# Performance work log

Measured on AMD Instinct MI355X. Metric: run time of the kernel, lower is better.

Reference implementation:

```python
import jax, jax.numpy as jnp
import numpy as np

N_NODES = 100000
M_HYPER = 50000
N_TOTAL = N_NODES + M_HYPER  # 150000
D_IN = 512
H_LAT = 256
N_CLASS = 40
NNZ = 4800000
NUM_LAYERS = 3


def setup_inputs() -> dict:
    key = jax.random.key(0)
    ks = jax.random.split(key, 8)
    X = jax.random.normal(ks[0], (N_TOTAL, D_IN), dtype=jnp.float32)
    W_red = jax.random.normal(ks[1], (D_IN, H_LAT), dtype=jnp.float32) / np.sqrt(D_IN)
    b_red = jax.random.normal(ks[2], (H_LAT,), dtype=jnp.float32) * 0.01
    W_cls = jax.random.normal(ks[3], (H_LAT, N_CLASS), dtype=jnp.float32) / np.sqrt(H_LAT)
    b_cls = jax.random.normal(ks[4], (N_CLASS,), dtype=jnp.float32) * 0.01
    # COO sparse normalized graph: value ~ 1/degree scale (avg_degree=32)
    edge_rows = jax.random.randint(ks[5], (NNZ,), 0, N_TOTAL, dtype=jnp.int32)
    edge_cols = jax.random.randint(ks[6], (NNZ,), 0, N_TOTAL, dtype=jnp.int32)
    edge_vals = jax.random.uniform(ks[7], (NNZ,), dtype=jnp.float32) * (1.0 / 32.0)
    return {
        "X": X, "W_red": W_red, "b_red": b_red,
        "W_cls": W_cls, "b_cls": b_cls,
        "edge_vals": edge_vals, "edge_rows": edge_rows, "edge_cols": edge_cols,
    }


def _spmm(edge_vals, edge_rows, edge_cols, emb):
    # out[r] = sum_{e: rows[e]==r} vals[e] * emb[cols[e]]
    msgs = edge_vals[:, None] * emb[edge_cols]  # [NNZ, H]
    return jax.ops.segment_sum(msgs, edge_rows, num_segments=N_TOTAL)


def reference(X, W_red, b_red, W_cls, b_cls, edge_vals, edge_rows, edge_cols):
    # reduction layer (dropout is identity in eval mode)
    emb = X @ W_red + b_red  # [N_TOTAL, H]
    # LightGCN-style propagation with running mean over layer outputs
    acc = emb
    cur = emb
    for _ in range(NUM_LAYERS):
        cur = _spmm(edge_vals, edge_rows, edge_cols, cur)
        acc = acc + cur
    out = acc / (NUM_LAYERS + 1)
    nodes = out[:N_NODES]  # split: nodes vs hyperedges
    Z = nodes @ W_cls + b_cls  # [N_NODES, C]
    return jax.nn.log_softmax(Z, axis=1)
```

## Files before the change

### kernel.cpp

```cpp
#include <hip/hip_runtime.h>

#define N_NODES 100000
#define M_HYPER 50000
#define N_TOTAL 150000
#define D_IN    512
#define H_LAT   256
#define N_CLASS 40
#define NNZ_E   4800000
#define CNT_PAD 151552
#define BK      128
#define BROWS   256
#define NB      ((N_TOTAL + BROWS - 1) / BROWS)
#define CH      4096
#define CLS_FB  16

#define S_EMB   16.0f
#define SP_OUT  8.0f
#define INV1    (1.0f / 128.0f)
#define INV2    (1.0f / 1024.0f)
#define INV3    (1.0f / 8192.0f)

typedef float  floatx4 __attribute__((ext_vector_type(4)));
typedef float  floatx2 __attribute__((ext_vector_type(2)));
typedef __bf16 bf16x8  __attribute__((ext_vector_type(8)));

__device__ __forceinline__ unsigned short bf16_rne(float f) {
    unsigned u = __float_as_uint(f);
    return (unsigned short)((u + 0x7FFFu + ((u >> 16) & 1u)) >> 16);
}
__device__ __forceinline__ float blo(unsigned w) { return __uint_as_float(w << 16); }
__device__ __forceinline__ float bhi(unsigned w) { return __uint_as_float(w & 0xFFFF0000u); }

__device__ __forceinline__ unsigned pack4fp8(float f0, float f1, float f2, float f3) {
    int d = __builtin_amdgcn_cvt_pk_fp8_f32(f0, f1, 0, false);
    d = __builtin_amdgcn_cvt_pk_fp8_f32(f2, f3, d, true);
    return (unsigned)d;
}

__global__ void __launch_bounds__(256) prep_wt_kernel(const float* __restrict__ W,
                                                      unsigned short* __restrict__ WT) {
    int t = blockIdx.x * 256 + threadIdx.x;
    if (t < D_IN * H_LAT) {
        int k = t >> 8;
        int n = t & 255;
        WT[n * D_IN + k] = bf16_rne(W[t]);
    }
}

__global__ void __launch_bounds__(256, 2) gemm1_kernel(const float* __restrict__ X,
                                                       const unsigned short* __restrict__ WT,
                                                       const float* __restrict__ brd,
                                                       unsigned short* __restrict__ emb,
                                                       unsigned char* __restrict__ emb8) {
    __shared__ __align__(16) unsigned short smem[64 * (H_LAT + 8)];
    unsigned short (*As)[BK + 8]    = (unsigned short (*)[BK + 8])smem;
    unsigned short (*Cs)[H_LAT + 8] = (unsigned short (*)[H_LAT + 8])smem;

    int tid  = threadIdx.x;
    int wv   = tid >> 6;
    int lane = tid & 63;
    int l16  = lane & 15;
    int quad = lane >> 4;
    int row0 = blockIdx.x * 64;

    int cst = (tid & 31) << 2;
    int rst = tid >> 5;
    const float* xbase = X + cst;

    float4 pf[8];
#pragma unroll
    for (int j = 0; j < 8; ++j) {
        int gr = min(row0 + rst + 8 * j, N_TOTAL - 1);
        pf[j] = *(const float4*)(xbase + (size_t)gr * D_IN);
    }

    floatx4 acc[4][4];
#pragma unroll
    for (int a = 0; a < 4; ++a)
#pragma unroll
        for (int b = 0; b < 4; ++b) acc[a][b] = (floatx4)0.f;

#pragma unroll 1
    for (int k0 = 0; k0 < D_IN; k0 += BK) {
#pragma unroll
        for (int j = 0; j < 8; ++j) {
            ushort4 u;
            u.x = bf16_rne(pf[j].x); u.y = bf16_rne(pf[j].y);
            u.z = bf16_rne(pf[j].z); u.w = bf16_rne(pf[j].w);
            *(ushort4*)(&As[rst + 8 * j][cst]) = u;
        }
        __syncthreads();

        bf16x8 bw[4][4];
#pragma unroll
        for (int s = 0; s < 4; ++s)
#pragma unroll
            for (int ct = 0; ct < 4; ++ct) {
                int col = wv * 64 + ct * 16 + l16;
                bw[s][ct] = *(const bf16x8*)(WT + (size_t)col * D_IN + k0 + s * 32 + quad * 8);
            }
        asm volatile("" ::: "memory");

        if (k0 + BK < D_IN) {
#pragma unroll
            for (int j = 0; j < 8; ++j) {
                int gr = min(row0 + rst + 8 * j, N_TOTAL - 1);
                pf[j] = *(const float4*)(xbase + (size_t)gr * D_IN + k0 + BK);
            }
        }
        asm volatile("" ::: "memory");

#pragma unroll
        for (int s = 0; s < 4; ++s) {
            int ks = s * 32;
            bf16x8 af[4];
#pragma unroll
            for (int rt = 0; rt < 4; ++rt)
                af[rt] = *(const bf16x8*)(&As[rt * 16 + l16][ks + quad * 8]);
#pragma unroll
            for (int ct = 0; ct < 4; ++ct) {
#pragma unroll
                for (int rt = 0; rt < 4; ++rt)
                    acc[rt][ct] = __builtin_amdgcn_mfma_f32_16x16x32_bf16(af[rt], bw[s][ct], acc[rt][ct], 0, 0, 0);
            }
        }
        __syncthreads();
    }

#pragma unroll
    for (int ct = 0; ct < 4; ++ct) {
        int col = wv * 64 + ct * 16 + l16;
        float bias = brd[col];
#pragma unroll
        for (int rt = 0; rt < 4; ++rt)
#pragma unroll
            for (int r = 0; r < 4; ++r)
                Cs[rt * 16 + quad * 4 + r][col] = bf16_rne(acc[rt][ct][r] + bias);
    }
    __syncthreads();

    int nbf = N_NODES - row0;
#pragma unroll
    for (int j = 0; j < 8; ++j) {
        int idx = tid + 256 * j;
        int r = idx >> 5;
        int cq = (idx & 31) * 8;
        if (r < nbf)
            *(uint4*)(emb + (size_t)(row0 + r) * H_LAT + cq) = *(const uint4*)(&Cs[r][cq]);
    }
#pragma unroll
    for (int j = 0; j < 4; ++j) {
        int idx = tid + 256 * j;
        int r = idx >> 4;
        int cq = (idx & 15) * 16;
        if (row0 + r < N_TOTAL) {
            const unsigned short* s = &Cs[r][cq];
            uint4 w0 = *(const uint4*)s;
            uint4 w1 = *(const uint4*)(s + 8);
            uint4 o;
            o.x = pack4fp8(S_EMB * blo(w0.x), S_EMB * bhi(w0.x), S_EMB * blo(w0.y), S_EMB * bhi(w0.y));
            o.y = pack4fp8(S_EMB * blo(w0.z), S_EMB * bhi(w0.z), S_EMB * blo(w0.w), S_EMB * bhi(w0.w));
            o.z = pack4fp8(S_EMB * blo(w1.x), S_EMB * bhi(w1.x), S_EMB * blo(w1.y), S_EMB * bhi(w1.y));
            o.w = pack4fp8(S_EMB * blo(w1.z), S_EMB * bhi(w1.z), S_EMB * blo(w1.w), S_EMB * bhi(w1.w));
            *(uint4*)(emb8 + (size_t)(row0 + r) * H_LAT + cq) = o;
        }
    }
}

__global__ void __launch_bounds__(256) bcnt_kernel(const int* __restrict__ rows,
                                                   int* __restrict__ bcnt) {
    __shared__ int h[NB];
    int tid = threadIdx.x;
    for (int i = tid; i < NB; i += 256) h[i] = 0;
    __syncthreads();
    long base = (long)blockIdx.x * (CH / 4);
    const int4* r4 = (const int4*)rows;
#pragma unroll
    for (int j = 0; j < 4; ++j) {
        long e = base + j * 256 + tid;
        if (e < NNZ_E / 4) {
            int4 r = r4[e];
            atomicAdd(&h[r.x >> 8], 1);
            atomicAdd(&h[r.y >> 8], 1);
            atomicAdd(&h[r.z >> 8], 1);
            atomicAdd(&h[r.w >> 8], 1);
        }
    }
    __syncthreads();
    for (int i = tid; i < NB; i += 256) {
        int c = h[i];
        if (c) atomicAdd(&bcnt[i], c);
    }
}

__global__ void __launch_bounds__(1024) bscan_kernel(const int* __restrict__ bcnt,
                                                     int* __restrict__ bptr,
                                                     int* __restrict__ bucket_fill) {
    __shared__ int ws[16];
    int tid = threadIdx.x;
    int lane = tid & 63, wid = tid >> 6;
    int v = (tid < NB) ? bcnt[tid] : 0;
    int s = v;
#pragma unroll
    for (int d = 1; d < 64; d <<= 1) {
        int o = __shfl_up(s, d);
        if (lane >= d) s += o;
    }
    if (lane == 63) ws[wid] = s;
    __syncthreads();
    if (wid == 0) {
        int w = (lane < 16) ? ws[lane] : 0;
#pragma unroll
        for (int d = 1; d < 16; d <<= 1) {
            int o = __shfl_up(w, d);
            if (lane >= d) w += o;
        }
        if (lane < 16) ws[lane] = w;
    }
    __syncthreads();
    int excl = s - v + ((wid > 0) ? ws[wid - 1] : 0);
    if (tid < NB) {
        bptr[tid] = excl;
        bucket_fill[tid] = excl;
    }
    if (tid == 0) bptr[NB] = NNZ_E;
}

__global__ void __launch_bounds__(256) binA_kernel(const int* __restrict__ rows,
                                                   const int* __restrict__ cols,
                                                   const float* __restrict__ vals,
                                                   int* __restrict__ bucket_fill,
                                                   int2* __restrict__ binned) {
    __shared__ int hist[NB];
    int tid = threadIdx.x;
    long base = (long)blockIdx.x * CH;
    for (int i = tid; i < NB; i += 256) hist[i] = 0;
    __syncthreads();

    int mybkt[16];
    int myrl[16];
#pragma unroll
    for (int j = 0; j < 16; ++j) {
        long e = base + j * 256 + tid;
        int b = -1, rl = 0;
        if (e < NNZ_E) {
            int r = rows[e];
            b = r >> 8;
            rl = r & 255;
            atomicAdd(&hist[b], 1);
        }
        mybkt[j] = b; myrl[j] = rl;
    }
    __syncthreads();
    for (int b = tid; b < NB; b += 256) {
        int c = hist[b];
        int g = 0;
        if (c > 0) g = atomicAdd(&bucket_fill[b], c);
        hist[b] = g;
    }
    __syncthreads();
#pragma unroll
    for (int j = 0; j < 16; ++j) {
        long e = base + j * 256 + tid;
        if (e < NNZ_E) {
            int b = mybkt[j];
            int pos = atomicAdd(&hist[b], 1);
            int c = cols[e];
            float v = vals[e];
            binned[pos] = make_int2(c | (myrl[j] << 18), __float_as_int(v));
        }
    }
}

__global__ void __launch_bounds__(256) binB_kernel(const int* __restrict__ bptr,
                                                   const int2* __restrict__ binned,
                                                   int* __restrict__ row_ptr,
                                                   int2* __restrict__ csr_ev) {
    __shared__ int lh[256];
    __shared__ int lofs[256];
    __shared__ int wsum[4];
    int b = blockIdx.x;
    int tid = threadIdx.x;
    int s = bptr[b], e = bptr[b + 1];

    lh[tid] = 0;
    __syncthreads();
    for (int t = s + tid; t < e; t += 256)
        atomicAdd(&lh[((unsigned)binned[t].x) >> 18], 1);
    __syncthreads();

    int v = lh[tid];
    int lane = tid & 63, wid = tid >> 6;
    int sc = v;
#pragma unroll
    for (int d = 1; d < 64; d <<= 1) {
        int o = __shfl_up(sc, d);
        if (lane >= d) sc += o;
    }
    if (lane == 63) wsum[wid] = sc;
    __syncthreads();
    int woff = 0;
    if (wid > 0) woff = wsum[0];
    if (wid > 1) woff += wsum[1];
    if (wid > 2) woff += wsum[2];
    int excl = sc - v + woff;
    lofs[tid] = s + excl;
    row_ptr[b * BROWS + tid] = s + excl;
    __syncthreads();

    for (int t = s + tid; t < e; t += 256) {
        int2 w = binned[t];
        int rl  = ((unsigned)w.x) >> 18;
        int col = w.x & 0x3FFFF;
        int p = atomicAdd(&lofs[rl], 1);
        csr_ev[p] = make_int2(col, w.y);
    }
}

__global__ void __launch_bounds__(256) spmm8_kernel(const unsigned char* __restrict__ cin8,
                                                    unsigned char* __restrict__ cout8,
                                                    const int* __restrict__ row_ptr,
                                                    const int2* __restrict__ csr_ev,
                                                    int nrows) {
    int r = (blockIdx.x * 256 + threadIdx.x) >> 6;
    if (r >= nrows) return;
    int lane = threadIdx.x & 63;
    int q   = lane >> 4;
    int l16 = lane & 15;
    int beg = row_ptr[r], end = row_ptr[r + 1];

    floatx2 a2[8];
#pragma unroll
    for (int j = 0; j < 8; ++j) a2[j] = (floatx2)0.f;
    const unsigned char* basep = cin8 + l16 * 16;

    for (int b = beg; b < end; b += 64) {
        int e = b + lane;
        int2 ev = (e < end) ? csr_ev[e] : make_int2(0, 0);
        int n = min(64, end - b);
        for (int i = 0; i < n; i += 16) {
            int cc[4]; float vv[4]; uint4 g[4];
#pragma unroll
            for (int u = 0; u < 4; ++u) {
                int src = i + 4 * u + q;
                cc[u] = __shfl(ev.x, src);
                vv[u] = __uint_as_float((unsigned)__shfl(ev.y, src));
            }
#pragma unroll
            for (int u = 0; u < 4; ++u) {
                if (i + 4 * u < n) g[u] = *(const uint4*)(basep + (size_t)cc[u] * H_LAT);
                else               g[u] = make_uint4(0, 0, 0, 0);
            }
#pragma unroll
            for (int u = 0; u < 4; ++u) {
                floatx2 vv2 = (floatx2)vv[u];
                a2[0] += vv2 * __builtin_amdgcn_cvt_pk_f32_fp8(g[u].x, false);
                a2[1] += vv2 * __builtin_amdgcn_cvt_pk_f32_fp8(g[u].x, true);
                a2[2] += vv2 * __builtin_amdgcn_cvt_pk_f32_fp8(g[u].y, false);
                a2[3] += vv2 * __builtin_amdgcn_cvt_pk_f32_fp8(g[u].y, true);
                a2[4] += vv2 * __builtin_amdgcn_cvt_pk_f32_fp8(g[u].z, false);
                a2[5] += vv2 * __builtin_amdgcn_cvt_pk_f32_fp8(g[u].z, true);
                a2[6] += vv2 * __builtin_amdgcn_cvt_pk_f32_fp8(g[u].w, false);
                a2[7] += vv2 * __builtin_amdgcn_cvt_pk_f32_fp8(g[u].w, true);
            }
        }
    }
#pragma unroll
    for (int j = 0; j < 8; ++j) {
#pragma unroll
        for (int k = 0; k < 2; ++k) {
            a2[j][k] += __shfl_xor(a2[j][k], 16);
            a2[j][k] += __shfl_xor(a2[j][k], 32);
        }
    }
    if (q == 0) {
        uint4 o;
        o.x = pack4fp8(SP_OUT * a2[0][0], SP_OUT * a2[0][1], SP_OUT * a2[1][0], SP_OUT * a2[1][1]);
        o.y = pack4fp8(SP_OUT * a2[2][0], SP_OUT * a2[2][1], SP_OUT * a2[3][0], SP_OUT * a2[3][1]);
        o.z = pack4fp8(SP_OUT * a2[4][0], SP_OUT * a2[4][1], SP_OUT * a2[5][0], SP_OUT * a2[5][1]);
        o.w = pack4fp8(SP_OUT * a2[6][0], SP_OUT * a2[6][1], SP_OUT * a2[7][0], SP_OUT * a2[7][1]);
        *(uint4*)(cout8 + (size_t)r * H_LAT + l16 * 16) = o;
    }
}

__global__ void __launch_bounds__(256, 2) cls_kernel(const unsigned short* __restrict__ emb,
                                                     const unsigned char* __restrict__ c1,
                                                     const unsigned char* __restrict__ c2,
                                                     const unsigned char* __restrict__ c3,
                                                     const float* __restrict__ W,
                                                     const float* __restrict__ bc,
                                                     float* __restrict__ out) {
    __shared__ float Wl[H_LAT * N_CLASS];
    __shared__ float bl[N_CLASS];
    __shared__ __align__(16) unsigned short embs[256][24];
    __shared__ __align__(16) unsigned char  c1s[256][32];
    __shared__ __align__(16) unsigned char  c2s[256][32];
    __shared__ __align__(16) unsigned char  c3s[256][32];

    int tid = threadIdx.x;
    for (int i = tid; i < H_LAT * N_CLASS; i += 256) Wl[i] = W[i];
    if (tid < N_CLASS) bl[tid] = bc[tid];
    __syncthreads();

    int row0 = blockIdx.x * 256;
    int r = row0 + tid;
    bool active = (r < N_NODES);

    floatx2 Z2[N_CLASS / 2];
#pragma unroll
    for (int c = 0; c < N_CLASS / 2; ++c) {
        Z2[c][0] = bl[2 * c];
        Z2[c][1] = bl[2 * c + 1];
    }

    int erow  = tid >> 1;
    int ehalf = tid & 1;
    int grc = min(r, N_NODES - 1);

#pragma unroll 1
    for (int f0 = 0; f0 < H_LAT; f0 += CLS_FB) {
#pragma unroll
        for (int j = 0; j < 2; ++j) {
            int rr = erow + 128 * j;
            int gr = min(row0 + rr, N_NODES - 1);
            *(uint4*)(&embs[rr][ehalf * 8]) =
                *(const uint4*)(emb + (size_t)gr * H_LAT + f0 + ehalf * 8);
        }
        {
            uint4 g1 = *(const uint4*)(c1 + (size_t)grc * H_LAT + f0);
            uint4 g2 = *(const uint4*)(c2 + (size_t)grc * H_LAT + f0);
            uint4 g3 = *(const uint4*)(c3 + (size_t)grc * H_LAT + f0);
            *(uint2*)(&c1s[tid][0]) = make_uint2(g1.x, g1.y);
            *(uint2*)(&c1s[tid][8]) = make_uint2(g1.z, g1.w);
            *(uint2*)(&c2s[tid][0]) = make_uint2(g2.x, g2.y);
            *(uint2*)(&c2s[tid][8]) = make_uint2(g2.z, g2.w);
            *(uint2*)(&c3s[tid][0]) = make_uint2(g3.x, g3.y);
            *(uint2*)(&c3s[tid][8]) = make_uint2(g3.z, g3.w);
        }
        __syncthreads();

        if (active) {
#pragma unroll
            for (int fg = 0; fg < CLS_FB; fg += 8) {
                int f = f0 + fg;
                uint4 ge = *(const uint4*)(&embs[tid][fg]);
                uint2 h1 = *(const uint2*)(&c1s[tid][fg]);
                uint2 h2 = *(const uint2*)(&c2s[tid][fg]);
                uint2 h3 = *(const uint2*)(&c3s[tid][fg]);
                float af[8];
                floatx2 pa, pb, pc;
                pa = __builtin_amdgcn_cvt_pk_f32_fp8(h1.x, false);
                pb = __builtin_amdgcn_cvt_pk_f32_fp8(h2.x, false);
                pc = __builtin_amdgcn_cvt_pk_f32_fp8(h3.x, false);
                af[0] = 0.25f * (blo(ge.x) + pa[0] * INV1 + pb[0] * INV2 + pc[0] * INV3);
                af[1] = 0.25f * (bhi(ge.x) + pa[1] * INV1 + pb[1] * INV2 + pc[1] * INV3);
                pa = __builtin_amdgcn_cvt_pk_f32_fp8(h1.x, true);
                pb = __builtin_amdgcn_cvt_pk_f32_fp8(h2.x, true);
                pc = __builtin_amdgcn_cvt_pk_f32_fp8(h3.x, true);
                af[2] = 0.25f * (blo(ge.y) + pa[0] * INV1 + pb[0] * INV2 + pc[0] * INV3);
                af[3] = 0.25f * (bhi(ge.y) + pa[1] * INV1 + pb[1] * INV2 + pc[1] * INV3);
                pa = __builtin_amdgcn_cvt_pk_f32_fp8(h1.y, false);
                pb = __builtin_amdgcn_cvt_pk_f32_fp8(h2.y, false);
                pc = __builtin_amdgcn_cvt_pk_f32_fp8(h3.y, false);
                af[4] = 0.25f * (blo(ge.z) + pa[0] * INV1 + pb[0] * INV2 + pc[0] * INV3);
                af[5] = 0.25f * (bhi(ge.z) + pa[1] * INV1 + pb[1] * INV2 + pc[1] * INV3);
                pa = __builtin_amdgcn_cvt_pk_f32_fp8(h1.y, true);
                pb = __builtin_amdgcn_cvt_pk_f32_fp8(h2.y, true);
                pc = __builtin_amdgcn_cvt_pk_f32_fp8(h3.y, true);
                af[6] = 0.25f * (blo(ge.w) + pa[0] * INV1 + pb[0] * INV2 + pc[0] * INV3);
                af[7] = 0.25f * (bhi(ge.w) + pa[1] * INV1 + pb[1] * INV2 + pc[1] * INV3);
#pragma unroll
                for (int j = 0; j < 8; ++j) {
                    const floatx2* wrow2 = (const floatx2*)&Wl[(f + j) * N_CLASS];
                    floatx2 af2 = (floatx2)af[j];
#pragma unroll
                    for (int c = 0; c < N_CLASS / 2; ++c) Z2[c] += af2 * wrow2[c];
                }
            }
        }
        __syncthreads();
    }

    if (!active) return;

    float m = fmaxf(Z2[0][0], Z2[0][1]);
#pragma unroll
    for (int c = 1; c < N_CLASS / 2; ++c) m = fmaxf(m, fmaxf(Z2[c][0], Z2[c][1]));
    float s = 0.f;
#pragma unroll
    for (int c = 0; c < N_CLASS / 2; ++c) s += __expf(Z2[c][0] - m) + __expf(Z2[c][1] - m);
    float ls = __logf(s) + m;
#pragma unroll
    for (int c = 0; c < N_CLASS / 2; ++c) {
        out[(size_t)r * N_CLASS + 2 * c]     = Z2[c][0] - ls;
        out[(size_t)r * N_CLASS + 2 * c + 1] = Z2[c][1] - ls;
    }
}

extern "C" void kernel_launch(void* const* d_in, const int* in_sizes, int n_in,
                              void* d_out, int out_size, void* d_ws, size_t ws_size,
                              hipStream_t stream) {
    const float* X        = (const float*)d_in[0];
    const float* W_red    = (const float*)d_in[1];
    const float* b_red    = (const float*)d_in[2];
    const float* W_cls    = (const float*)d_in[3];
    const float* b_cls    = (const float*)d_in[4];
    const float* e_vals   = (const float*)d_in[5];
    const int*   e_rows   = (const int*)d_in[6];
    const int*   e_cols   = (const int*)d_in[7];
    float* out = (float*)d_out;

    char* p = (char*)d_ws;
    auto carve = [&](size_t bytes) -> void* {
        void* r = (void*)p;
        p += (bytes + 255) & ~(size_t)255;
        return r;
    };
    unsigned short* WT   = (unsigned short*)carve((size_t)H_LAT * D_IN * 2);
    unsigned short* emb  = (unsigned short*)carve((size_t)N_TOTAL * H_LAT * 2);
    unsigned char*  emb8 = (unsigned char*)carve((size_t)N_TOTAL * H_LAT);
    unsigned char*  c1_8 = (unsigned char*)carve((size_t)N_TOTAL * H_LAT);
    unsigned char*  c2_8 = (unsigned char*)carve((size_t)N_TOTAL * H_LAT);
    unsigned char*  c3_8 = (unsigned char*)carve((size_t)N_TOTAL * H_LAT);
    int*   row_ptr     = (int*)carve((size_t)CNT_PAD * 4);
    int*   bcnt        = (int*)carve((size_t)NB * 4);
    int*   bptr        = (int*)carve((size_t)(NB + 1) * 4);
    int*   bucket_fill = (int*)carve((size_t)NB * 4);
    int2*  csr_ev      = (int2*)carve((size_t)NNZ_E * 8);
    int2*  binned      = (int2*)c2_8;

    hipMemsetAsync(bcnt, 0, (size_t)NB * 4, stream);

    prep_wt_kernel<<<512, 256, 0, stream>>>(W_red, WT);
    gemm1_kernel<<<(N_TOTAL + 63) / 64, 256, 0, stream>>>(X, WT, b_red, emb, emb8);

    bcnt_kernel<<<(NNZ_E + CH - 1) / CH, 256, 0, stream>>>(e_rows, bcnt);
    bscan_kernel<<<1, 1024, 0, stream>>>(bcnt, bptr, bucket_fill);
    binA_kernel<<<(NNZ_E + CH - 1) / CH, 256, 0, stream>>>(e_rows, e_cols, e_vals, bucket_fill, binned);
    binB_kernel<<<NB, 256, 0, stream>>>(bptr, binned, row_ptr, csr_ev);

    spmm8_kernel<<<N_TOTAL / 4, 256, 0, stream>>>(emb8, c1_8, row_ptr, csr_ev, N_TOTAL);
    spmm8_kernel<<<N_TOTAL / 4, 256, 0, stream>>>(c1_8, c2_8, row_ptr, csr_ev, N_TOTAL);
    spmm8_kernel<<<N_NODES / 4, 256, 0, stream>>>(c2_8, c3_8, row_ptr, csr_ev, N_NODES);

    cls_kernel<<<(N_NODES + 255) / 256, 256, 0, stream>>>(emb, c1_8, c2_8, c3_8, W_cls, b_cls, out);
}
```

Measured before the change: 1.216 ms.

## Software-pipeline SpMM gathers and split GEMM weight loads to raise occupancy

In the SpMM kernel, the gathers for the next 16 edges are issued before the FMAs on the current batch run, so memory latency overlaps with compute. In the reduction GEMM, the per-tile weight fragments are loaded in two halves instead of all at once, which lowers register pressure, and launch bounds are raised to target three blocks per CU. The SpMM change adds live registers for the double buffer, and the extra occupancy hint may cause spills in the GEMM.

New measurement: 1.273 ms. 1.05x slower.

```diff
diff --git a/kernel.cpp b/kernel.cpp
--- a/kernel.cpp
+++ b/kernel.cpp
@@ -20,6 +20,7 @@
 #define INV2    (1.0f / 1024.0f)
 #define INV3    (1.0f / 8192.0f)
 
+
 typedef float  floatx4 __attribute__((ext_vector_type(4)));
 typedef float  floatx2 __attribute__((ext_vector_type(2)));
 typedef __bf16 bf16x8  __attribute__((ext_vector_type(8)));
@@ -47,7 +48,7 @@
     }
 }
 
-__global__ void __launch_bounds__(256, 2) gemm1_kernel(const float* __restrict__ X,
+__global__ void __launch_bounds__(256, 3) gemm1_kernel(const float* __restrict__ X,
                                                        const unsigned short* __restrict__ WT,
                                                        const float* __restrict__ brd,
                                                        unsigned short* __restrict__ emb,
@@ -91,13 +92,13 @@
         }
         __syncthreads();
 
-        bf16x8 bw[4][4];
-#pragma unroll
-        for (int s = 0; s < 4; ++s)
+        bf16x8 bwA[2][4];
+#pragma unroll
+        for (int s = 0; s < 2; ++s)
 #pragma unroll
             for (int ct = 0; ct < 4; ++ct) {
                 int col = wv * 64 + ct * 16 + l16;
-                bw[s][ct] = *(const bf16x8*)(WT + (size_t)col * D_IN + k0 + s * 32 + quad * 8);
+                bwA[s][ct] = *(const bf16x8*)(WT + (size_t)col * D_IN + k0 + s * 32 + quad * 8);
             }
         asm volatile("" ::: "memory");
 
@@ -111,7 +112,7 @@
         asm volatile("" ::: "memory");
 
 #pragma unroll
-        for (int s = 0; s < 4; ++s) {
+        for (int s = 0; s < 2; ++s) {
             int ks = s * 32;
             bf16x8 af[4];
 #pragma unroll
@@ -121,7 +122,33 @@
             for (int ct = 0; ct < 4; ++ct) {
 #pragma unroll
                 for (int rt = 0; rt < 4; ++rt)
-                    acc[rt][ct] = __builtin_amdgcn_mfma_f32_16x16x32_bf16(af[rt], bw[s][ct], acc[rt][ct], 0, 0, 0);
+                    acc[rt][ct] = __builtin_amdgcn_mfma_f32_16x16x32_bf16(af[rt], bwA[s][ct], acc[rt][ct], 0, 0, 0);
+            }
+        }
+        asm volatile("" ::: "memory");
+
+        bf16x8 bwB[2][4];
+#pragma unroll
+        for (int s = 0; s < 2; ++s)
+#pragma unroll
+            for (int ct = 0; ct < 4; ++ct) {
+                int col = wv * 64 + ct * 16 + l16;
+                bwB[s][ct] = *(const bf16x8*)(WT + (size_t)col * D_IN + k0 + (s + 2) * 32 + quad * 8);
+            }
+        asm volatile("" ::: "memory");
+
+#pragma unroll
+        for (int s = 0; s < 2; ++s) {
+            int ks = (s + 2) * 32;
+            bf16x8 af[4];
+#pragma unroll
+            for (int rt = 0; rt < 4; ++rt)
+                af[rt] = *(const bf16x8*)(&As[rt * 16 + l16][ks + quad * 8]);
+#pragma unroll
+            for (int ct = 0; ct < 4; ++ct) {
+#pragma unroll
+                for (int rt = 0; rt < 4; ++rt)
+                    acc[rt][ct] = __builtin_amdgcn_mfma_f32_16x16x32_bf16(af[rt], bwB[s][ct], acc[rt][ct], 0, 0, 0);
             }
         }
         __syncthreads();
@@ -338,18 +365,39 @@
         int e = b + lane;
         int2 ev = (e < end) ? csr_ev[e] : make_int2(0, 0);
         int n = min(64, end - b);
+
+        float vv[4]; uint4 g[4];
+        {
+            int cc0[4];
+#pragma unroll
+            for (int u = 0; u < 4; ++u) {
+                int src = 4 * u + q;
+                cc0[u] = __shfl(ev.x, src);
+                vv[u]  = __uint_as_float((unsigned)__shfl(ev.y, src));
+            }
+#pragma unroll
+            for (int u = 0; u < 4; ++u) {
+                if (4 * u < n) g[u] = *(const uint4*)(basep + (size_t)cc0[u] * H_LAT);
+                else           g[u] = make_uint4(0, 0, 0, 0);
+            }
+        }
+
         for (int i = 0; i < n; i += 16) {
-            int cc[4]; float vv[4]; uint4 g[4];
-#pragma unroll
-            for (int u = 0; u < 4; ++u) {
-                int src = i + 4 * u + q;
-                cc[u] = __shfl(ev.x, src);
-                vv[u] = __uint_as_float((unsigned)__shfl(ev.y, src));
-            }
-#pragma unroll
-            for (int u = 0; u < 4; ++u) {
-                if (i + 4 * u < n) g[u] = *(const uint4*)(basep + (size_t)cc[u] * H_LAT);
-                else               g[u] = make_uint4(0, 0, 0, 0);
+            bool more = (i + 16) < n;
+            float vvn[4]; uint4 gn[4];
+            if (more) {
+                int ccn[4];
+#pragma unroll
+                for (int u = 0; u < 4; ++u) {
+                    int src = i + 16 + 4 * u + q;
+                    ccn[u] = __shfl(ev.x, src);
+                    vvn[u] = __uint_as_float((unsigned)__shfl(ev.y, src));
+                }
+#pragma unroll
+                for (int u = 0; u < 4; ++u) {
+                    if (i + 16 + 4 * u < n) gn[u] = *(const uint4*)(basep + (size_t)ccn[u] * H_LAT);
+                    else                    gn[u] = make_uint4(0, 0, 0, 0);
+                }
             }
 #pragma unroll
             for (int u = 0; u < 4; ++u) {
@@ -362,6 +410,10 @@
                 a2[5] += vv2 * __builtin_amdgcn_cvt_pk_f32_fp8(g[u].z, true);
                 a2[6] += vv2 * __builtin_amdgcn_cvt_pk_f32_fp8(g[u].w, false);
                 a2[7] += vv2 * __builtin_amdgcn_cvt_pk_f32_fp8(g[u].w, true);
+            }
+            if (more) {
+#pragma unroll
+                for (int u = 0; u < 4; ++u) { g[u] = gn[u]; vv[u] = vvn[u]; }
             }
         }
     }
```
